# Optimization experiments

Measured on AMD Instinct MI355X. Metric: run time of the kernel, lower is better.

## Reference

```python
import jax, jax.numpy as jnp
import numpy as np

NUM_MODES = 64
NUM_KNOTS = 8
NUM_STEPS = 80
B = 8192


def setup_inputs() -> dict:
    key = jax.random.key(0)
    k1, k2, k3, k4, k5 = jax.random.split(key, 5)
    inputs = jax.random.normal(k1, (B, NUM_MODES + NUM_MODES * NUM_KNOTS * 2), dtype=jnp.float32)
    x = jax.random.normal(k2, (B, 1), dtype=jnp.float32)
    y = jax.random.normal(k3, (B, 1), dtype=jnp.float32)
    yaw = jax.random.normal(k4, (B, 1), dtype=jnp.float32)
    centroids = jax.random.normal(k5, (NUM_MODES, NUM_STEPS * 2), dtype=jnp.float32)
    return {"inputs": inputs, "x": x, "y": y, "yaw": yaw, "centroids": centroids}


def _cubic_bspline_basis(t):
    # t in [0,1); tensorflow_graphics cubic B-spline basis, shape t.shape + (4,)
    t2 = t * t
    t3 = t2 * t
    b0 = (1.0 - t) ** 3 / 6.0
    b1 = (3.0 * t3 - 6.0 * t2 + 4.0) / 6.0
    b2 = (-3.0 * t3 + 3.0 * t2 + 3.0 * t + 1.0) / 6.0
    b3 = t3 / 6.0
    return jnp.stack([b0, b1, b2, b3], axis=-1)


def reference(inputs, x, y, yaw, centroids):
    M, C, T = NUM_MODES, NUM_KNOTS, NUM_STEPS
    confidences = jax.nn.softmax(inputs[:, :M], axis=-1)  # (B, M)
    knots = inputs[:, M:].reshape(-1, M, 2, C)  # (B, M, 2, C)

    # positions = arange(0, C-3, (C-3)/T) -> T values in [0, C-3)
    max_pos = float(C - 3)
    pos = jnp.arange(T, dtype=knots.dtype) * (max_pos / T)  # (T,)
    shift = jnp.floor(pos).astype(jnp.int32)  # (T,)
    basis = _cubic_bspline_basis(pos - shift)  # (T, 4)

    # sparse gather of the 4 active knots per position (equivalent to full
    # num_knots weight vector in tfg.bspline.interpolate, non-cyclical)
    idx = shift[:, None] + jnp.arange(4, dtype=jnp.int32)[None, :]  # (T, 4)
    gathered = knots[..., idx]  # (B, M, 2, T, 4)
    spline = jnp.einsum('bmdtk,tk->bmtd', gathered, basis)  # (B, M, T, 2)

    pred = spline + centroids.reshape(1, M, T, 2)  # centroid bias

    c = jnp.cos(yaw)  # (B, 1)
    s = jnp.sin(yaw)
    flat = pred.reshape(-1, M * T, 2)
    px = c * flat[..., 0] - s * flat[..., 1] + x
    py = s * flat[..., 0] + c * flat[..., 1] + y
    pred = jnp.stack([px, py], axis=-1).reshape(-1, M, T, 2)
    return pred, confidences, knots
```

## Files before the change

### kernel.cpp

```cpp
#include <hip/hip_runtime.h>
#include <math.h>

#define NMODES 64
#define NKNOTS 8
#define NSTEPS 80
#define ROW    1088
#define PREDF  10240

typedef float f4 __attribute__((ext_vector_type(4)));

__launch_bounds__(256, 4)
__global__ void head_kernel(const float* __restrict__ inputs,
                            const float* __restrict__ x,
                            const float* __restrict__ y,
                            const float* __restrict__ yaw,
                            const float* __restrict__ centroids,
                            float* __restrict__ pred,
                            float* __restrict__ conf,
                            float* __restrict__ knots_out)
{
    __shared__ float s_kn[NMODES * NKNOTS * 2];
    __shared__ float s_rot[4];

    const int tid = threadIdx.x;
    const int b   = blockIdx.x;

    const f4* row4 = (const f4*)(inputs + (size_t)b * ROW);
    f4 kv = row4[16 + tid];
    __builtin_nontemporal_store(kv, (f4*)(knots_out + (size_t)b * 1024) + tid);
    {
        int g = tid * 4;
        #pragma unroll
        for (int e = 0; e < 4; ++e) {
            int gg = g + e;
            int m  = gg >> 4;
            int rr = gg & 15;
            int d  = rr >> 3;
            int c  = rr & 7;
            s_kn[(m << 4) + (c << 1) + d] = kv[e];
        }
    }

    if (tid == 0) {
        float sy, cy;
        sincosf(yaw[b], &sy, &cy);
        s_rot[0] = cy;  s_rot[1] = sy;
        s_rot[2] = x[b]; s_rot[3] = y[b];
    }

    if (tid < 64) {
        float v  = inputs[(size_t)b * ROW + tid];
        float mx = v;
        #pragma unroll
        for (int off = 32; off > 0; off >>= 1)
            mx = fmaxf(mx, __shfl_xor(mx, off));
        float e = expf(v - mx);
        float sum = e;
        #pragma unroll
        for (int off = 32; off > 0; off >>= 1)
            sum += __shfl_xor(sum, off);
        __builtin_nontemporal_store(e / sum, conf + (size_t)b * NMODES + tid);
    }

    __syncthreads();

    const float rc = s_rot[0], rs = s_rot[1], X = s_rot[2], Y = s_rot[3];
    const f4* cent4 = (const f4*)centroids;
    f4* out4 = (f4*)(pred + (size_t)b * PREDF);

    int m   = (tid * 205) >> 13;
    int r   = tid - m * 40;
    int idx = tid;

    #pragma unroll 2
    for (int j = 0; j < 10; ++j) {
        const int   sh = r >> 3;
        const float u0 = (float)(r & 7) * 0.125f;
        const float u1 = u0 + 0.0625f;

        const float2* kp = (const float2*)(s_kn + (m << 4) + (sh << 1));
        float2 k0 = kp[0], k1 = kp[1], k2 = kp[2], k3 = kp[3];

        f4 cent = cent4[idx];
        f4 o;
        {
            float u2 = u0 * u0, u3 = u2 * u0, omu = 1.0f - u0;
            float b0 = omu * omu * omu * (1.0f / 6.0f);
            float b1 = 0.5f * u3 - u2 + (2.0f / 3.0f);
            float b2 = -0.5f * u3 + 0.5f * u2 + 0.5f * u0 + (1.0f / 6.0f);
            float b3 = u3 * (1.0f / 6.0f);
            float fx = b0 * k0.x + b1 * k1.x + b2 * k2.x + b3 * k3.x + cent.x;
            float fy = b0 * k0.y + b1 * k1.y + b2 * k2.y + b3 * k3.y + cent.y;
            o.x = rc * fx - rs * fy + X;
            o.y = rs * fx + rc * fy + Y;
        }
        {
            float u2 = u1 * u1, u3 = u2 * u1, omu = 1.0f - u1;
            float b0 = omu * omu * omu * (1.0f / 6.0f);
            float b1 = 0.5f * u3 - u2 + (2.0f / 3.0f);
            float b2 = -0.5f * u3 + 0.5f * u2 + 0.5f * u1 + (1.0f / 6.0f);
            float b3 = u3 * (1.0f / 6.0f);
            float fx = b0 * k0.x + b1 * k1.x + b2 * k2.x + b3 * k3.x + cent.z;
            float fy = b0 * k0.y + b1 * k1.y + b2 * k2.y + b3 * k3.y + cent.w;
            o.z = rc * fx - rs * fy + X;
            o.w = rs * fx + rc * fy + Y;
        }
        __builtin_nontemporal_store(o, out4 + idx);

        idx += 256;
        r += 16; m += 6;
        if (r >= 40) { r -= 40; ++m; }
    }
}

extern "C" void kernel_launch(void* const* d_in, const int* in_sizes, int n_in,
                              void* d_out, int out_size, void* d_ws, size_t ws_size,
                              hipStream_t stream)
{
    const float* inputs    = (const float*)d_in[0];
    const float* x         = (const float*)d_in[1];
    const float* y         = (const float*)d_in[2];
    const float* yaw       = (const float*)d_in[3];
    const float* centroids = (const float*)d_in[4];

    const int B = in_sizes[1];

    float* pred      = (float*)d_out;
    float* conf      = pred + (size_t)B * NMODES * NSTEPS * 2;
    float* knots_out = conf + (size_t)B * NMODES;

    head_kernel<<<B, 256, 0, stream>>>(inputs, x, y, yaw, centroids,
                                       pred, conf, knots_out);
}
```

Before: 403.8 us.

## Process four batch rows per block, reusing basis weights and centroid loads

```diff
diff --git a/kernel.cpp b/kernel.cpp
--- a/kernel.cpp
+++ b/kernel.cpp
@@ -6,6 +6,7 @@
 #define NSTEPS 80
 #define ROW    1088
 #define PREDF  10240
+#define RPB    4
 
 typedef float f4 __attribute__((ext_vector_type(4)));
 
@@ -19,93 +20,113 @@
                             float* __restrict__ conf,
                             float* __restrict__ knots_out)
 {
-    __shared__ float s_kn[NMODES * NKNOTS * 2];
-    __shared__ float s_rot[4];
+    __shared__ float s_kn[RPB][NMODES * NKNOTS * 2];
+    __shared__ float s_rot[RPB][4];
 
-    const int tid = threadIdx.x;
-    const int b   = blockIdx.x;
+    const int    tid = threadIdx.x;
+    const size_t b0  = (size_t)blockIdx.x * RPB;
 
-    const f4* row4 = (const f4*)(inputs + (size_t)b * ROW);
-    f4 kv = row4[16 + tid];
-    __builtin_nontemporal_store(kv, (f4*)(knots_out + (size_t)b * 1024) + tid);
-    {
-        int g = tid * 4;
+    f4    kv[RPB];
+    float cv[RPB];
+    #pragma unroll
+    for (int k = 0; k < RPB; ++k) {
+        const float* rowp = inputs + (b0 + k) * ROW;
+        kv[k] = ((const f4*)rowp)[16 + tid];
+        cv[k] = (tid < 64) ? rowp[tid] : 0.0f;
+    }
+    if (tid < RPB) {
+        float sy, cw;
+        sincosf(yaw[b0 + tid], &sy, &cw);
+        s_rot[tid][0] = cw;          s_rot[tid][1] = sy;
+        s_rot[tid][2] = x[b0 + tid]; s_rot[tid][3] = y[b0 + tid];
+    }
+    #pragma unroll
+    for (int k = 0; k < RPB; ++k) {
+        const int g = tid * 4;
         #pragma unroll
         for (int e = 0; e < 4; ++e) {
-            int gg = g + e;
-            int m  = gg >> 4;
-            int rr = gg & 15;
-            int d  = rr >> 3;
-            int c  = rr & 7;
-            s_kn[(m << 4) + (c << 1) + d] = kv[e];
+            const int gg = g + e;
+            s_kn[k][((gg >> 4) << 4) + ((gg & 7) << 1) + ((gg >> 3) & 1)] = kv[k][e];
+        }
+    }
+    __syncthreads();
+
+    #pragma unroll
+    for (int k = 0; k < RPB; ++k)
+        __builtin_nontemporal_store(kv[k], (f4*)(knots_out + (b0 + k) * 1024) + tid);
+
+    if (tid < 64) {
+        #pragma unroll
+        for (int k = 0; k < RPB; ++k) {
+            float v = cv[k], mx = v;
+            #pragma unroll
+            for (int off = 32; off > 0; off >>= 1)
+                mx = fmaxf(mx, __shfl_xor(mx, off));
+            float e = expf(v - mx), sum = e;
+            #pragma unroll
+            for (int off = 32; off > 0; off >>= 1)
+                sum += __shfl_xor(sum, off);
+            __builtin_nontemporal_store(e / sum, conf + (b0 + k) * NMODES + tid);
         }
     }
 
-    if (tid == 0) {
-        float sy, cy;
-        sincosf(yaw[b], &sy, &cy);
-        s_rot[0] = cy;  s_rot[1] = sy;
-        s_rot[2] = x[b]; s_rot[3] = y[b];
+    float rc[RPB], rs[RPB], Xo[RPB], Yo[RPB];
+    #pragma unroll
+    for (int k = 0; k < RPB; ++k) {
+        rc[k] = s_rot[k][0]; rs[k] = s_rot[k][1];
+        Xo[k] = s_rot[k][2]; Yo[k] = s_rot[k][3];
     }
 
-    if (tid < 64) {
-        float v  = inputs[(size_t)b * ROW + tid];
-        float mx = v;
-        #pragma unroll
-        for (int off = 32; off > 0; off >>= 1)
-            mx = fmaxf(mx, __shfl_xor(mx, off));
-        float e = expf(v - mx);
-        float sum = e;
-        #pragma unroll
-        for (int off = 32; off > 0; off >>= 1)
-            sum += __shfl_xor(sum, off);
-        __builtin_nontemporal_store(e / sum, conf + (size_t)b * NMODES + tid);
-    }
-
-    __syncthreads();
-
-    const float rc = s_rot[0], rs = s_rot[1], X = s_rot[2], Y = s_rot[3];
     const f4* cent4 = (const f4*)centroids;
-    f4* out4 = (f4*)(pred + (size_t)b * PREDF);
 
     int m   = (tid * 205) >> 13;
     int r   = tid - m * 40;
     int idx = tid;
 
-    #pragma unroll 2
+    #pragma unroll
     for (int j = 0; j < 10; ++j) {
         const int   sh = r >> 3;
         const float u0 = (float)(r & 7) * 0.125f;
         const float u1 = u0 + 0.0625f;
 
-        const float2* kp = (const float2*)(s_kn + (m << 4) + (sh << 1));
-        float2 k0 = kp[0], k1 = kp[1], k2 = kp[2], k3 = kp[3];
-
-        f4 cent = cent4[idx];
-        f4 o;
+        float w0[4], w1[4];
         {
             float u2 = u0 * u0, u3 = u2 * u0, omu = 1.0f - u0;
-            float b0 = omu * omu * omu * (1.0f / 6.0f);
-            float b1 = 0.5f * u3 - u2 + (2.0f / 3.0f);
-            float b2 = -0.5f * u3 + 0.5f * u2 + 0.5f * u0 + (1.0f / 6.0f);
-            float b3 = u3 * (1.0f / 6.0f);
-            float fx = b0 * k0.x + b1 * k1.x + b2 * k2.x + b3 * k3.x + cent.x;
-            float fy = b0 * k0.y + b1 * k1.y + b2 * k2.y + b3 * k3.y + cent.y;
-            o.x = rc * fx - rs * fy + X;
-            o.y = rs * fx + rc * fy + Y;
+            w0[0] = omu * omu * omu * (1.0f / 6.0f);
+            w0[1] = 0.5f * u3 - u2 + (2.0f / 3.0f);
+            w0[2] = -0.5f * u3 + 0.5f * u2 + 0.5f * u0 + (1.0f / 6.0f);
+            w0[3] = u3 * (1.0f / 6.0f);
         }
         {
             float u2 = u1 * u1, u3 = u2 * u1, omu = 1.0f - u1;
-            float b0 = omu * omu * omu * (1.0f / 6.0f);
-            float b1 = 0.5f * u3 - u2 + (2.0f / 3.0f);
-            float b2 = -0.5f * u3 + 0.5f * u2 + 0.5f * u1 + (1.0f / 6.0f);
-            float b3 = u3 * (1.0f / 6.0f);
-            float fx = b0 * k0.x + b1 * k1.x + b2 * k2.x + b3 * k3.x + cent.z;
-            float fy = b0 * k0.y + b1 * k1.y + b2 * k2.y + b3 * k3.y + cent.w;
-            o.z = rc * fx - rs * fy + X;
-            o.w = rs * fx + rc * fy + Y;
+            w1[0] = omu * omu * omu * (1.0f / 6.0f);
+            w1[1] = 0.5f * u3 - u2 + (2.0f / 3.0f);
+            w1[2] = -0.5f * u3 + 0.5f * u2 + 0.5f * u1 + (1.0f / 6.0f);
+            w1[3] = u3 * (1.0f / 6.0f);
         }
-        __builtin_nontemporal_store(o, out4 + idx);
+
+        const f4  cent = cent4[idx];
+        const int kofs = (m << 4) + (sh << 1);
+
+        #pragma unroll
+        for (int k = 0; k < RPB; ++k) {
+            const float2* kp = (const float2*)(&s_kn[k][kofs]);
+            const float2 k0 = kp[0], k1 = kp[1], k2 = kp[2], k3 = kp[3];
+            f4 o;
+            {
+                float fx = w0[0]*k0.x + w0[1]*k1.x + w0[2]*k2.x + w0[3]*k3.x + cent.x;
+                float fy = w0[0]*k0.y + w0[1]*k1.y + w0[2]*k2.y + w0[3]*k3.y + cent.y;
+                o.x = rc[k] * fx - rs[k] * fy + Xo[k];
+                o.y = rs[k] * fx + rc[k] * fy + Yo[k];
+            }
+            {
+                float fx = w1[0]*k0.x + w1[1]*k1.x + w1[2]*k2.x + w1[3]*k3.x + cent.z;
+                float fy = w1[0]*k0.y + w1[1]*k1.y + w1[2]*k2.y + w1[3]*k3.y + cent.w;
+                o.z = rc[k] * fx - rs[k] * fy + Xo[k];
+                o.w = rs[k] * fx + rc[k] * fy + Yo[k];
+            }
+            __builtin_nontemporal_store(o, (f4*)(pred + (b0 + k) * PREDF) + idx);
+        }
 
         idx += 256;
         r += 16; m += 6;
@@ -129,6 +150,6 @@
     float* conf      = pred + (size_t)B * NMODES * NSTEPS * 2;
     float* knots_out = conf + (size_t)B * NMODES;
 
-    head_kernel<<<B, 256, 0, stream>>>(inputs, x, y, yaw, centroids,
-                                       pred, conf, knots_out);
+    head_kernel<<<B / RPB, 256, 0, stream>>>(inputs, x, y, yaw, centroids,
+                                             pred, conf, knots_out);
 }
```

After: 394.4 us. 1.02x faster.
